# Performance work log

Hardware: AMD Instinct MI355X
Metric: run time of the kernel (lower is better)

The kernel has to match this reference:

```python
import jax, jax.numpy as jnp
import numpy as np

D_MODEL = 1024
N_HEADS = 16
D_HEAD = D_MODEL // N_HEADS

def setup_inputs() -> dict:
    key = jax.random.key(0)
    kx, kq, kk, kv, ko = jax.random.split(key, 5)
    s = 1.0 / np.sqrt(D_MODEL)
    return {
        "x": jax.random.normal(kx, (4, 2048, D_MODEL), dtype=jnp.float32),
        "W_q": jax.random.normal(kq, (D_MODEL, D_MODEL), dtype=jnp.float32) * s,
        "W_k": jax.random.normal(kk, (D_MODEL, D_MODEL), dtype=jnp.float32) * s,
        "W_v": jax.random.normal(kv, (D_MODEL, D_MODEL), dtype=jnp.float32) * s,
        "W_o": jax.random.normal(ko, (D_MODEL, D_MODEL), dtype=jnp.float32) * s,
    }

def reference(x, W_q, W_k, W_v, W_o):
    B, L, _ = x.shape
    def heads(h):  # (B,L,D) -> (B,H,L,d_head)
        return h.reshape(B, L, N_HEADS, D_HEAD).transpose(0, 2, 1, 3)
    # nn.Linear: y = x @ W.T
    q = heads(x @ W_q.T)
    k = heads(x @ W_k.T)
    v = heads(x @ W_v.T)
    scores = jnp.einsum('bhqd,bhkd->bhqk', q, k) / jnp.sqrt(jnp.float32(D_HEAD))
    attn = jax.nn.softmax(scores, axis=-1)
    ctx = jnp.einsum('bhqk,bhkd->bhqd', attn, v)
    ctx = ctx.transpose(0, 2, 1, 3).reshape(B, L, D_MODEL)
    return ctx @ W_o.T
```

## Files before the change

kernel.cpp:

```cpp
#include <hip/hip_runtime.h>
#include <hip/hip_fp16.h>

typedef _Float16 f16;
typedef _Float16 f16x2 __attribute__((ext_vector_type(2)));
typedef _Float16 f16x4 __attribute__((ext_vector_type(4)));
typedef _Float16 f16x8 __attribute__((ext_vector_type(8)));
typedef float f32x4 __attribute__((ext_vector_type(4)));
typedef float f32x16 __attribute__((ext_vector_type(16)));

#define NHEADS 16
#define DHEAD 64
#define DM 1024
#define BATCH 4
#define SEQ 2048
#define MTOT (BATCH*SEQ)

__device__ inline void gload_lds16(const void* g, void* l) {
  __builtin_amdgcn_global_load_lds(
      (const __attribute__((address_space(1))) void*)g,
      (__attribute__((address_space(3))) void*)l, 16, 0, 0);
}

__device__ inline float max3f(float a, float b, float c) {
  return fmaxf(fmaxf(a, b), c);
}

__device__ inline unsigned pkrtz(float a, float b) {
  auto h = __builtin_amdgcn_cvt_pkrtz(a, b);
  unsigned u; __builtin_memcpy(&u, &h, 4); return u;
}

__global__ __launch_bounds__(256) void cvt_f32_f16_k(const float* __restrict__ s,
                                                     f16* __restrict__ d, int n) {
  int i = (blockIdx.x * 256 + threadIdx.x) * 8;
  if (i + 8 <= n) {
    float4 a = *reinterpret_cast<const float4*>(s + i);
    float4 b = *reinterpret_cast<const float4*>(s + i + 4);
    f16x8 h = {(f16)a.x,(f16)a.y,(f16)a.z,(f16)a.w,(f16)b.x,(f16)b.y,(f16)b.z,(f16)b.w};
    *reinterpret_cast<f16x8*>(d + i) = h;
  } else {
    for (int j = i; j < n; ++j) d[j] = (f16)s[j];
  }
}

__global__ __launch_bounds__(256) void cvt_w4_k(const float* __restrict__ w0,
                                                const float* __restrict__ w1,
                                                const float* __restrict__ w2,
                                                const float* __restrict__ w3,
                                                f16* __restrict__ d) {
  int which = blockIdx.x >> 9;
  const float* s = which == 0 ? w0 : which == 1 ? w1 : which == 2 ? w2 : w3;
  int off = ((blockIdx.x & 511) * 256 + threadIdx.x) * 8;
  float4 a = *reinterpret_cast<const float4*>(s + off);
  float4 b = *reinterpret_cast<const float4*>(s + off + 4);
  f16x8 h = {(f16)a.x,(f16)a.y,(f16)a.z,(f16)a.w,(f16)b.x,(f16)b.y,(f16)b.z,(f16)b.w};
  *reinterpret_cast<f16x8*>(d + (size_t)which * DM * DM + off) = h;
}

template <int MODE>
__device__ void gemm_nt_body(const f16* __restrict__ A, const f16* __restrict__ Bw,
                             void* __restrict__ outp, int n0, float oscale,
                             f16* Ah, f16* Bh) {
  const int tx = threadIdx.x;
  const int wave = tx >> 6, lane = tx & 63;
  const int m0 = blockIdx.y * 128;
  const int wm = (wave >> 1) * 64, wn = (wave & 1) * 64;

  f32x4 acc[4][4];
#pragma unroll
  for (int i = 0; i < 4; ++i)
#pragma unroll
    for (int j = 0; j < 4; ++j) acc[i][j] = {0.f, 0.f, 0.f, 0.f};

  const int srow = lane >> 2;
  const int scol = (lane & 3) * 8;

  for (int k0 = 0; k0 < DM; k0 += 32) {
    __syncthreads();
#pragma unroll
    for (int i = 0; i < 2; ++i) {
      int chunk = wave * 2 + i;
      gload_lds16(A  + (size_t)(m0 + chunk * 16 + srow) * DM + k0 + scol, Ah + chunk * 512);
      gload_lds16(Bw + (size_t)(n0 + chunk * 16 + srow) * DM + k0 + scol, Bh + chunk * 512);
    }
    __syncthreads();

    f16x8 af[4], bf[4];
#pragma unroll
    for (int i = 0; i < 4; ++i)
      af[i] = *reinterpret_cast<const f16x8*>(Ah + (wm + i * 16 + (lane & 15)) * 32 + (lane >> 4) * 8);
#pragma unroll
    for (int j = 0; j < 4; ++j)
      bf[j] = *reinterpret_cast<const f16x8*>(Bh + (wn + j * 16 + (lane & 15)) * 32 + (lane >> 4) * 8);
#pragma unroll
    for (int i = 0; i < 4; ++i)
#pragma unroll
      for (int j = 0; j < 4; ++j)
        acc[i][j] = __builtin_amdgcn_mfma_f32_16x16x32_f16(af[i], bf[j], acc[i][j], 0, 0, 0);
  }

  const int r0 = (lane >> 4) * 4, c0 = lane & 15;
#pragma unroll
  for (int i = 0; i < 4; ++i)
#pragma unroll
    for (int j = 0; j < 4; ++j)
#pragma unroll
      for (int r = 0; r < 4; ++r) {
        int gm = m0 + wm + i * 16 + r0 + r;
        int gn = n0 + wn + j * 16 + c0;
        float v = acc[i][j][r] * oscale;
        if (MODE == 2) {
          ((float*)outp)[(size_t)gm * DM + gn] = v;
        } else {
          int b = gm >> 11, l = gm & 2047, h = gn >> 6, d = gn & 63;
          size_t idx = (MODE == 0)
            ? (((size_t)(b * NHEADS + h) * SEQ + l) * DHEAD + d)
            : (((size_t)(b * NHEADS + h) * DHEAD + d) * SEQ + l);
          ((f16*)outp)[idx] = (f16)v;
        }
      }
}

__global__ __launch_bounds__(256) void gemm_qkv(const f16* __restrict__ xh,
                                                const f16* __restrict__ Wf,
                                                f16* __restrict__ Qb,
                                                f16* __restrict__ Kb,
                                                f16* __restrict__ VTb,
                                                float qscale) {
  __shared__ f16 Ah[128 * 32];
  __shared__ f16 Bh[128 * 32];
  int which = blockIdx.x >> 3;
  int n0 = (blockIdx.x & 7) * 128;
  const f16* Bw = Wf + (size_t)which * DM * DM;
  if (which == 0)      gemm_nt_body<0>(xh, Bw, Qb,  n0, qscale, Ah, Bh);
  else if (which == 1) gemm_nt_body<0>(xh, Bw, Kb,  n0, 1.0f,  Ah, Bh);
  else                 gemm_nt_body<1>(xh, Bw, VTb, n0, 1.0f,  Ah, Bh);
}

__global__ __launch_bounds__(256) void gemm_out(const f16* __restrict__ A,
                                                const f16* __restrict__ Bw,
                                                float* __restrict__ outp) {
  __shared__ f16 Ah[128 * 32];
  __shared__ f16 Bh[128 * 32];
  gemm_nt_body<2>(A, Bw, outp, blockIdx.x * 128, 1.0f, Ah, Bh);
}

__global__ __launch_bounds__(256, 4) void attn_k(const f16* __restrict__ Q,
                                                 const f16* __restrict__ Kg,
                                                 const f16* __restrict__ VT,
                                                 f16* __restrict__ ctx) {
  __shared__ f16 Kt[2][64 * 64];
  __shared__ f16 Vt[2][64 * 64];
  const int tx = threadIdx.x, wave = tx >> 6, lane = tx & 63;
  const int m = lane & 31, hi = lane >> 5, m7 = m & 7;
  const int bh = blockIdx.y;
  const int q0 = blockIdx.x * 128;
  const f16* Qb = Q  + (size_t)bh * SEQ * DHEAD;
  const f16* Kb = Kg + (size_t)bh * SEQ * DHEAD;
  const f16* Vb = VT + (size_t)bh * DHEAD * SEQ;

  const int gi0 = wave * 128 + lane, gi1 = gi0 + 64;
  const int r0s = gi0 >> 3, sc0 = (((gi0 & 7) ^ (r0s & 7))) * 8;
  const int r1s = gi1 >> 3, sc1 = (((gi1 & 7) ^ (r1s & 7))) * 8;

  auto stage = [&](int buf, int k0) {
    gload_lds16(Kb + (size_t)(k0 + r0s) * DHEAD + sc0, &Kt[buf][(size_t)(wave * 128) * 8]);
    gload_lds16(Kb + (size_t)(k0 + r1s) * DHEAD + sc1, &Kt[buf][(size_t)(wave * 128 + 64) * 8]);
    gload_lds16(Vb + (size_t)r0s * SEQ + k0 + sc0,     &Vt[buf][(size_t)(wave * 128) * 8]);
    gload_lds16(Vb + (size_t)r1s * SEQ + k0 + sc1,     &Vt[buf][(size_t)(wave * 128 + 64) * 8]);
  };

  f16x8 qb[4];
#pragma unroll
  for (int s = 0; s < 4; ++s)
    qb[s] = *reinterpret_cast<const f16x8*>(
        Qb + (size_t)(q0 + wave * 32 + m) * DHEAD + s * 16 + hi * 8);

  const f16x8 ones = {(f16)1, (f16)1, (f16)1, (f16)1, (f16)1, (f16)1, (f16)1, (f16)1};
  f32x16 oacc[2], lacc;
#pragma unroll
  for (int r = 0; r < 16; ++r) { oacc[0][r] = 0.f; oacc[1][r] = 0.f; lacc[r] = 0.f; }
  float mrun = -1e30f;

  auto compute = [&](const f16* Kc, const f16* Vc) {
    f32x16 st[2];
    __builtin_amdgcn_s_setprio(1);
#pragma unroll
    for (int kt = 0; kt < 2; ++kt) {
      f32x16 a;
#pragma unroll
      for (int r = 0; r < 16; ++r) a[r] = 0.f;
#pragma unroll
      for (int s = 0; s < 4; ++s) {
        f16x8 ka = *reinterpret_cast<const f16x8*>(
            Kc + ((kt * 32 + m) * 8 + ((2 * s + hi) ^ m7)) * 8);
        a = __builtin_amdgcn_mfma_f32_32x32x16_f16(ka, qb[s], a, 0, 0, 0);
      }
      st[kt] = a;
    }
    __builtin_amdgcn_s_setprio(0);

    float a0 = max3f(st[0][0], st[0][1], st[0][2]);
    float a1 = max3f(st[0][3], st[0][4], st[0][5]);
    float a2 = max3f(st[0][6], st[0][7], st[0][8]);
    float a3 = max3f(st[0][9], st[0][10], st[0][11]);
    float a4 = max3f(st[0][12], st[0][13], st[0][14]);
    float a5 = max3f(st[0][15], st[1][0], st[1][1]);
    float a6 = max3f(st[1][2], st[1][3], st[1][4]);
    float a7 = max3f(st[1][5], st[1][6], st[1][7]);
    float a8 = max3f(st[1][8], st[1][9], st[1][10]);
    float a9 = max3f(st[1][11], st[1][12], st[1][13]);
    float b0 = max3f(a0, a1, a2), b1 = max3f(a3, a4, a5);
    float b2 = max3f(a6, a7, a8), b3 = max3f(a9, st[1][14], st[1][15]);
    float mx = fmaxf(fmaxf(b0, b1), fmaxf(b2, b3));
    mx = fmaxf(mx, __shfl_xor(mx, 32));

    if (!__all(mx <= mrun + 8.f)) {
      float mnew = fmaxf(mrun, mx);
      float scl = __builtin_amdgcn_exp2f(mrun - mnew);
#pragma unroll
      for (int r = 0; r < 16; ++r) { oacc[0][r] *= scl; oacc[1][r] *= scl; lacc[r] *= scl; }
      mrun = mnew;
    }

    unsigned pk[2][8];
#pragma unroll
    for (int kt = 0; kt < 2; ++kt)
#pragma unroll
      for (int j = 0; j < 8; ++j)
        pk[kt][j] = pkrtz(__builtin_amdgcn_exp2f(st[kt][2 * j] - mrun),
                          __builtin_amdgcn_exp2f(st[kt][2 * j + 1] - mrun));

    __builtin_amdgcn_s_setprio(1);
#pragma unroll
    for (int c = 0; c < 4; ++c) {
      const int kt = c >> 1, c1 = c & 1;
      unsigned w0 = pk[kt][4 * c1 + 0], w1 = pk[kt][4 * c1 + 1];
      unsigned w2 = pk[kt][4 * c1 + 2], w3 = pk[kt][4 * c1 + 3];
      asm("v_permlane32_swap_b32 %0, %1" : "+v"(w0), "+v"(w2));
      asm("v_permlane32_swap_b32 %0, %1" : "+v"(w1), "+v"(w3));
      union { unsigned u[4]; f16x8 h; } pu;
      pu.u[0] = w0; pu.u[1] = w1; pu.u[2] = w2; pu.u[3] = w3;
      lacc = __builtin_amdgcn_mfma_f32_32x32x16_f16(ones, pu.h, lacc, 0, 0, 0);
#pragma unroll
      for (int dt = 0; dt < 2; ++dt) {
        f16x8 va = *reinterpret_cast<const f16x8*>(
            Vc + ((dt * 32 + m) * 8 + ((2 * c + hi) ^ m7)) * 8);
        oacc[dt] = __builtin_amdgcn_mfma_f32_32x32x16_f16(va, pu.h, oacc[dt], 0, 0, 0);
      }
    }
    __builtin_amdgcn_s_setprio(0);
  };

  stage(0, 0);
  __syncthreads();
  for (int tt = 0; tt < 32; tt += 2) {
    stage(1, (tt + 1) * 64);
    compute(Kt[0], Vt[0]);
    __syncthreads();
    if (tt + 2 < 32) stage(0, (tt + 2) * 64);
    compute(Kt[1], Vt[1]);
    __syncthreads();
  }

  const int b = bh >> 4, hd = bh & 15;
  const float inv = 1.0f / lacc[0];
  const int q = q0 + wave * 32 + m;
  f16* obase = ctx + ((size_t)b * SEQ + q) * DM + hd * DHEAD;
#pragma unroll
  for (int dt = 0; dt < 2; ++dt)
#pragma unroll
    for (int t = 0; t < 4; ++t) {
      f16x4 o = {(f16)(oacc[dt][4 * t + 0] * inv), (f16)(oacc[dt][4 * t + 1] * inv),
                 (f16)(oacc[dt][4 * t + 2] * inv), (f16)(oacc[dt][4 * t + 3] * inv)};
      *reinterpret_cast<f16x4*>(obase + dt * 32 + t * 8 + 4 * hi) = o;
    }
}

extern "C" void kernel_launch(void* const* d_in, const int* in_sizes, int n_in,
                              void* d_out, int out_size, void* d_ws, size_t ws_size,
                              hipStream_t stream) {
  (void)in_sizes; (void)n_in; (void)out_size; (void)ws_size;
  const float* x  = (const float*)d_in[0];
  const float* Wq = (const float*)d_in[1];
  const float* Wk = (const float*)d_in[2];
  const float* Wv = (const float*)d_in[3];
  const float* Wo = (const float*)d_in[4];

  char* ws = (char*)d_ws;
  const size_t SZ_X = (size_t)MTOT * DM * sizeof(f16);
  const size_t SZ_W = (size_t)DM * DM * sizeof(f16);
  f16* xh  = (f16*)(ws);
  f16* wfh = (f16*)(ws + SZ_X);
  f16* woh = (f16*)(ws + SZ_X + 3 * SZ_W);
  f16* Qb  = (f16*)(ws + 1 * SZ_X + 4 * SZ_W);
  f16* Kb  = (f16*)(ws + 2 * SZ_X + 4 * SZ_W);
  f16* VTb = (f16*)(ws + 3 * SZ_X + 4 * SZ_W);
  f16* ctx = xh;

  const int nx = MTOT * DM;
  const float QSCALE = 0.125f * 1.44269504088896f;

  cvt_f32_f16_k<<<nx / 2048, 256, 0, stream>>>(x, xh, nx);
  cvt_w4_k<<<2048, 256, 0, stream>>>(Wq, Wk, Wv, Wo, wfh);

  gemm_qkv<<<dim3(24, MTOT / 128), 256, 0, stream>>>(xh, wfh, Qb, Kb, VTb, QSCALE);

  attn_k<<<dim3(SEQ / 128, BATCH * NHEADS), 256, 0, stream>>>(Qb, Kb, VTb, ctx);

  gemm_out<<<dim3(DM / 128, MTOT / 128), 256, 0, stream>>>(ctx, woh, (float*)d_out);
}
```

Before: 225.3 us.

## Double-buffer GEMM LDS, swizzle attention blocks, compute row sums with fdot2

The GEMM body now double-buffers its A/B LDS tiles so the next k-slice loads while MFMAs run, with one barrier per iteration instead of two. The attention kernel remaps block IDs to group blocks that share a head, processes softmax per 32-key subtile instead of per 64-key tile, and replaces the row-sum MFMA with ones by fdot2 accumulation plus a final cross-half shuffle. These aim to hide global-load latency in the GEMMs, drop a quarter of the attention MFMAs, and improve cache locality. In exchange LDS use per GEMM block doubles and the max/rescale check runs twice as often.

```diff
diff --git a/kernel.cpp b/kernel.cpp
--- a/kernel.cpp
+++ b/kernel.cpp
@@ -28,6 +28,16 @@
 __device__ inline unsigned pkrtz(float a, float b) {
   auto h = __builtin_amdgcn_cvt_pkrtz(a, b);
   unsigned u; __builtin_memcpy(&u, &h, 4); return u;
+}
+
+__device__ inline float accum2(unsigned w, float acc) {
+  f16x2 p; __builtin_memcpy(&p, &w, 4);
+#if __has_builtin(__builtin_amdgcn_fdot2)
+  const f16x2 one2 = {(f16)1, (f16)1};
+  return __builtin_amdgcn_fdot2(p, one2, acc, false);
+#else
+  return acc + (float)p[0] + (float)p[1];
+#endif
 }
 
 __global__ __launch_bounds__(256) void cvt_f32_f16_k(const float* __restrict__ s,
@@ -75,28 +85,38 @@
   const int srow = lane >> 2;
   const int scol = (lane & 3) * 8;
 
-  for (int k0 = 0; k0 < DM; k0 += 32) {
-    __syncthreads();
+  auto stage = [&](int buf, int k0) {
 #pragma unroll
     for (int i = 0; i < 2; ++i) {
       int chunk = wave * 2 + i;
-      gload_lds16(A  + (size_t)(m0 + chunk * 16 + srow) * DM + k0 + scol, Ah + chunk * 512);
-      gload_lds16(Bw + (size_t)(n0 + chunk * 16 + srow) * DM + k0 + scol, Bh + chunk * 512);
+      gload_lds16(A  + (size_t)(m0 + chunk * 16 + srow) * DM + k0 + scol,
+                  Ah + buf * 4096 + chunk * 512);
+      gload_lds16(Bw + (size_t)(n0 + chunk * 16 + srow) * DM + k0 + scol,
+                  Bh + buf * 4096 + chunk * 512);
     }
-    __syncthreads();
-
+  };
+
+  stage(0, 0);
+  __syncthreads();
+  for (int k0 = 0; k0 < DM; k0 += 32) {
+    const int cur = (k0 >> 5) & 1;
+    if (k0 + 32 < DM) stage(cur ^ 1, k0 + 32);
+
+    const f16* Ac = Ah + cur * 4096;
+    const f16* Bc = Bh + cur * 4096;
     f16x8 af[4], bf[4];
 #pragma unroll
     for (int i = 0; i < 4; ++i)
-      af[i] = *reinterpret_cast<const f16x8*>(Ah + (wm + i * 16 + (lane & 15)) * 32 + (lane >> 4) * 8);
+      af[i] = *reinterpret_cast<const f16x8*>(Ac + (wm + i * 16 + (lane & 15)) * 32 + (lane >> 4) * 8);
 #pragma unroll
     for (int j = 0; j < 4; ++j)
-      bf[j] = *reinterpret_cast<const f16x8*>(Bh + (wn + j * 16 + (lane & 15)) * 32 + (lane >> 4) * 8);
+      bf[j] = *reinterpret_cast<const f16x8*>(Bc + (wn + j * 16 + (lane & 15)) * 32 + (lane >> 4) * 8);
 #pragma unroll
     for (int i = 0; i < 4; ++i)
 #pragma unroll
       for (int j = 0; j < 4; ++j)
         acc[i][j] = __builtin_amdgcn_mfma_f32_16x16x32_f16(af[i], bf[j], acc[i][j], 0, 0, 0);
+    __syncthreads();
   }
 
   const int r0 = (lane >> 4) * 4, c0 = lane & 15;
@@ -127,8 +147,8 @@
                                                 f16* __restrict__ Kb,
                                                 f16* __restrict__ VTb,
                                                 float qscale) {
-  __shared__ f16 Ah[128 * 32];
-  __shared__ f16 Bh[128 * 32];
+  __shared__ f16 Ah[2 * 128 * 32];
+  __shared__ f16 Bh[2 * 128 * 32];
   int which = blockIdx.x >> 3;
   int n0 = (blockIdx.x & 7) * 128;
   const f16* Bw = Wf + (size_t)which * DM * DM;
@@ -140,8 +160,8 @@
 __global__ __launch_bounds__(256) void gemm_out(const f16* __restrict__ A,
                                                 const f16* __restrict__ Bw,
                                                 float* __restrict__ outp) {
-  __shared__ f16 Ah[128 * 32];
-  __shared__ f16 Bh[128 * 32];
+  __shared__ f16 Ah[2 * 128 * 32];
+  __shared__ f16 Bh[2 * 128 * 32];
   gemm_nt_body<2>(A, Bw, outp, blockIdx.x * 128, 1.0f, Ah, Bh);
 }
 
@@ -153,8 +173,12 @@
   __shared__ f16 Vt[2][64 * 64];
   const int tx = threadIdx.x, wave = tx >> 6, lane = tx & 63;
   const int m = lane & 31, hi = lane >> 5, m7 = m & 7;
-  const int bh = blockIdx.y;
-  const int q0 = blockIdx.x * 128;
+
+  const int bid = blockIdx.y * 16 + blockIdx.x;
+  const int swz = (bid & 7) * 128 + (bid >> 3);
+  const int bh = swz >> 4;
+  const int q0 = (swz & 15) * 128;
+
   const f16* Qb = Q  + (size_t)bh * SEQ * DHEAD;
   const f16* Kb = Kg + (size_t)bh * SEQ * DHEAD;
   const f16* Vb = VT + (size_t)bh * DHEAD * SEQ;
@@ -176,80 +200,71 @@
     qb[s] = *reinterpret_cast<const f16x8*>(
         Qb + (size_t)(q0 + wave * 32 + m) * DHEAD + s * 16 + hi * 8);
 
-  const f16x8 ones = {(f16)1, (f16)1, (f16)1, (f16)1, (f16)1, (f16)1, (f16)1, (f16)1};
-  f32x16 oacc[2], lacc;
-#pragma unroll
-  for (int r = 0; r < 16; ++r) { oacc[0][r] = 0.f; oacc[1][r] = 0.f; lacc[r] = 0.f; }
+  f32x16 oacc[2];
+#pragma unroll
+  for (int r = 0; r < 16; ++r) { oacc[0][r] = 0.f; oacc[1][r] = 0.f; }
+  float lsum = 0.f;
   float mrun = -1e30f;
 
   auto compute = [&](const f16* Kc, const f16* Vc) {
-    f32x16 st[2];
-    __builtin_amdgcn_s_setprio(1);
 #pragma unroll
     for (int kt = 0; kt < 2; ++kt) {
-      f32x16 a;
-#pragma unroll
-      for (int r = 0; r < 16; ++r) a[r] = 0.f;
+      f32x16 st;
+#pragma unroll
+      for (int r = 0; r < 16; ++r) st[r] = 0.f;
+      __builtin_amdgcn_s_setprio(1);
 #pragma unroll
       for (int s = 0; s < 4; ++s) {
         f16x8 ka = *reinterpret_cast<const f16x8*>(
             Kc + ((kt * 32 + m) * 8 + ((2 * s + hi) ^ m7)) * 8);
-        a = __builtin_amdgcn_mfma_f32_32x32x16_f16(ka, qb[s], a, 0, 0, 0);
+        st = __builtin_amdgcn_mfma_f32_32x32x16_f16(ka, qb[s], st, 0, 0, 0);
       }
-      st[kt] = a;
+      __builtin_amdgcn_s_setprio(0);
+
+      float a0 = max3f(st[0], st[1], st[2]);
+      float a1 = max3f(st[3], st[4], st[5]);
+      float a2 = max3f(st[6], st[7], st[8]);
+      float a3 = max3f(st[9], st[10], st[11]);
+      float a4 = max3f(st[12], st[13], st[14]);
+      float mx = fmaxf(fmaxf(max3f(a0, a1, a2), fmaxf(a3, a4)), st[15]);
+      mx = fmaxf(mx, __shfl_xor(mx, 32));
+
+      if (!__all(mx <= mrun + 8.f)) {
+        float mnew = fmaxf(mrun, mx);
+        float scl = __builtin_amdgcn_exp2f(mrun - mnew);
+#pragma unroll
+        for (int r = 0; r < 16; ++r) { oacc[0][r] *= scl; oacc[1][r] *= scl; }
+        lsum *= scl;
+        mrun = mnew;
+      }
+
+      unsigned pk[8];
+#pragma unroll
+      for (int j = 0; j < 8; ++j)
+        pk[j] = pkrtz(__builtin_amdgcn_exp2f(st[2 * j] - mrun),
+                      __builtin_amdgcn_exp2f(st[2 * j + 1] - mrun));
+#pragma unroll
+      for (int j = 0; j < 8; ++j) lsum = accum2(pk[j], lsum);
+
+      __builtin_amdgcn_s_setprio(1);
+#pragma unroll
+      for (int c1 = 0; c1 < 2; ++c1) {
+        const int c = kt * 2 + c1;
+        unsigned w0 = pk[4 * c1 + 0], w1 = pk[4 * c1 + 1];
+        unsigned w2 = pk[4 * c1 + 2], w3 = pk[4 * c1 + 3];
+        asm("v_permlane32_swap_b32 %0, %1" : "+v"(w0), "+v"(w2));
+        asm("v_permlane32_swap_b32 %0, %1" : "+v"(w1), "+v"(w3));
+        union { unsigned u[4]; f16x8 h; } pu;
+        pu.u[0] = w0; pu.u[1] = w1; pu.u[2] = w2; pu.u[3] = w3;
+#pragma unroll
+        for (int dt = 0; dt < 2; ++dt) {
+          f16x8 va = *reinterpret_cast<const f16x8*>(
+              Vc + ((dt * 32 + m) * 8 + ((2 * c + hi) ^ m7)) * 8);
+          oacc[dt] = __builtin_amdgcn_mfma_f32_32x32x16_f16(va, pu.h, oacc[dt], 0, 0, 0);
+        }
+      }
+      __builtin_amdgcn_s_setprio(0);
     }
-    __builtin_amdgcn_s_setprio(0);
-
-    float a0 = max3f(st[0][0], st[0][1], st[0][2]);
-    float a1 = max3f(st[0][3], st[0][4], st[0][5]);
-    float a2 = max3f(st[0][6], st[0][7], st[0][8]);
-    float a3 = max3f(st[0][9], st[0][10], st[0][11]);
-    float a4 = max3f(st[0][12], st[0][13], st[0][14]);
-    float a5 = max3f(st[0][15], st[1][0], st[1][1]);
-    float a6 = max3f(st[1][2], st[1][3], st[1][4]);
-    float a7 = max3f(st[1][5], st[1][6], st[1][7]);
-    float a8 = max3f(st[1][8], st[1][9], st[1][10]);
-    float a9 = max3f(st[1][11], st[1][12], st[1][13]);
-    float b0 = max3f(a0, a1, a2), b1 = max3f(a3, a4, a5);
-    float b2 = max3f(a6, a7, a8), b3 = max3f(a9, st[1][14], st[1][15]);
-    float mx = fmaxf(fmaxf(b0, b1), fmaxf(b2, b3));
-    mx = fmaxf(mx, __shfl_xor(mx, 32));
-
-    if (!__all(mx <= mrun + 8.f)) {
-      float mnew = fmaxf(mrun, mx);
-      float scl = __builtin_amdgcn_exp2f(mrun - mnew);
-#pragma unroll
-      for (int r = 0; r < 16; ++r) { oacc[0][r] *= scl; oacc[1][r] *= scl; lacc[r] *= scl; }
-      mrun = mnew;
-    }
-
-    unsigned pk[2][8];
-#pragma unroll
-    for (int kt = 0; kt < 2; ++kt)
-#pragma unroll
-      for (int j = 0; j < 8; ++j)
-        pk[kt][j] = pkrtz(__builtin_amdgcn_exp2f(st[kt][2 * j] - mrun),
-                          __builtin_amdgcn_exp2f(st[kt][2 * j + 1] - mrun));
-
-    __builtin_amdgcn_s_setprio(1);
-#pragma unroll
-    for (int c = 0; c < 4; ++c) {
-      const int kt = c >> 1, c1 = c & 1;
-      unsigned w0 = pk[kt][4 * c1 + 0], w1 = pk[kt][4 * c1 + 1];
-      unsigned w2 = pk[kt][4 * c1 + 2], w3 = pk[kt][4 * c1 + 3];
-      asm("v_permlane32_swap_b32 %0, %1" : "+v"(w0), "+v"(w2));
-      asm("v_permlane32_swap_b32 %0, %1" : "+v"(w1), "+v"(w3));
-      union { unsigned u[4]; f16x8 h; } pu;
-      pu.u[0] = w0; pu.u[1] = w1; pu.u[2] = w2; pu.u[3] = w3;
-      lacc = __builtin_amdgcn_mfma_f32_32x32x16_f16(ones, pu.h, lacc, 0, 0, 0);
-#pragma unroll
-      for (int dt = 0; dt < 2; ++dt) {
-        f16x8 va = *reinterpret_cast<const f16x8*>(
-            Vc + ((dt * 32 + m) * 8 + ((2 * c + hi) ^ m7)) * 8);
-        oacc[dt] = __builtin_amdgcn_mfma_f32_32x32x16_f16(va, pu.h, oacc[dt], 0, 0, 0);
-      }
-    }
-    __builtin_amdgcn_s_setprio(0);
   };
 
   stage(0, 0);
@@ -263,8 +278,9 @@
     __syncthreads();
   }
 
+  const float ltot = lsum + __shfl_xor(lsum, 32);
+  const float inv = 1.0f / ltot;
   const int b = bh >> 4, hd = bh & 15;
-  const float inv = 1.0f / lacc[0];
   const int q = q0 + wave * 32 + m;
   f16* obase = ctx + ((size_t)b * SEQ + q) * DM + hd * DHEAD;
 #pragma unroll
```

Result: faster. 205.3 us (-8.9%).
